# Kernel optimization log

Hardware: AMD Instinct MI355X
Metric: run time of the kernel (lower is better)

Reference implementation:

```python
import jax, jax.numpy as jnp
import numpy as np

B, T, C, A, H = 2048, 2048, 8, 27, 8  # batch, timesteps, conv in-channels, n attrs, hidden nodes
KEEP = 0.9  # dropout rate 0.1


def setup_inputs() -> dict:
    key = jax.random.key(0)
    ks = jax.random.split(key, 10)
    uni = lambda k, s: jax.random.uniform(k, s, jnp.float32, -0.05, 0.05)  # keras RandomUniform default
    # inverted dropout masks (values 0 or 1/keep); the original reuses the same seed
    # for both attrs dropouts and the same seed for both hidden dropouts -> shared masks
    mask_attrs = jax.random.bernoulli(ks[8], KEEP, (B, A)).astype(jnp.float32) / KEEP
    mask_hidden = jax.random.bernoulli(ks[9], KEEP, (B, H)).astype(jnp.float32) / KEEP
    return {
        "x": jax.random.normal(ks[0], (B, T, C), jnp.float32),
        "attrs": jax.random.normal(ks[1], (B, A), jnp.float32),
        "c2_weight_w1": uni(ks[2], (A, H)),
        "c2_weight_b1": jnp.zeros((H,), jnp.float32),
        "c2_weight_w2": uni(ks[3], (H, C)),
        "c2_weight_b2": jnp.zeros((C,), jnp.float32),
        "c2_bias_w1": uni(ks[4], (A, H)),
        "c2_bias_b1": jnp.zeros((H,), jnp.float32),
        "c2_bias_w2": uni(ks[5], (H, 1)),
        "c2_bias_b2": jnp.zeros((1,), jnp.float32),
        "mask_attrs": mask_attrs,
        "mask_hidden": mask_hidden,
    }


def reference(x, attrs, c2_weight_w1, c2_weight_b1, c2_weight_w2, c2_weight_b2,
              c2_bias_w1, c2_bias_b1, c2_bias_w2, c2_bias_b2,
              mask_attrs, mask_hidden):
    a = attrs * mask_attrs  # [B, A] shared dropout (same seed in both branches)
    # per-sample conv kernel (kernel_size=1, so just a [B, C] vector)
    hw = jax.nn.relu(a @ c2_weight_w1 + c2_weight_b1) * mask_hidden  # [B, H]
    kernel = jnp.tanh(hw @ c2_weight_w2 + c2_weight_b2)              # [B, C]
    # per-sample bias
    hb = jax.nn.relu(a @ c2_bias_w1 + c2_bias_b1) * mask_hidden      # [B, H]
    bias = jnp.tanh(hb @ c2_bias_w2 + c2_bias_b2)                    # [B, 1]
    # kernel-size-1 valid conv == per-sample channel contraction, batched across B
    y = jnp.einsum('btc,bc->bt', x, kernel) + bias                   # [B, T]
    return jax.nn.elu(y)[..., None]                                  # [B, T, 1]
```

## Files before the change

kernel.cpp:

```cpp
#include <hip/hip_runtime.h>

#define BB 2048
#define TT 2048
#define CC 8
#define AA 27
#define HH 8

__global__ __launch_bounds__(256) void mlp_kernel(
    const float* __restrict__ attrs,
    const float* __restrict__ w1,
    const float* __restrict__ b1,
    const float* __restrict__ w2,
    const float* __restrict__ b2,
    const float* __restrict__ bw1,
    const float* __restrict__ bb1,
    const float* __restrict__ bw2,
    const float* __restrict__ bb2,
    const float* __restrict__ mask_attrs,
    const float* __restrict__ mask_hidden,
    float* __restrict__ ker,
    float* __restrict__ bias)
{
    const int tid = threadIdx.x;
    const int s   = tid >> 3;
    const int h   = tid & 7;
    const int b   = blockIdx.x * 32 + s;

    __shared__ float s_hw[32][HH];
    __shared__ float s_hb[32][HH];

    {
        float hw = b1[h];
        float hb = bb1[h];
        const float* ab = attrs      + b * AA;
        const float* mb = mask_attrs + b * AA;
        #pragma unroll
        for (int i = 0; i < AA; ++i) {
            const float a = ab[i] * mb[i];
            hw = fmaf(a, w1 [i * HH + h], hw);
            hb = fmaf(a, bw1[i * HH + h], hb);
        }
        const float mh = mask_hidden[b * HH + h];
        s_hw[s][h] = fmaxf(hw, 0.0f) * mh;
        s_hb[s][h] = fmaxf(hb, 0.0f) * mh;
    }
    __syncthreads();

    {
        const int c = h;
        float acc = b2[c];
        #pragma unroll
        for (int j = 0; j < HH; ++j)
            acc = fmaf(s_hw[s][j], w2[j * CC + c], acc);
        ker[b * CC + c] = tanhf(acc);
        if (c == 0) {
            float accb = bb2[0];
            #pragma unroll
            for (int j = 0; j < HH; ++j)
                accb = fmaf(s_hb[s][j], bw2[j], accb);
            bias[b] = tanhf(accb);
        }
    }
}

__global__ __launch_bounds__(256) void stream_kernel(
    const float* __restrict__ x,
    const float* __restrict__ ker,
    const float* __restrict__ bias,
    float* __restrict__ out)
{
    const int idx = blockIdx.x * 256 + threadIdx.x;
    const int b   = idx >> 11;

    const float4* xp = reinterpret_cast<const float4*>(x + (size_t)idx * CC);
    const float4 x0 = xp[0];
    const float4 x1 = xp[1];

    const float4* kp = reinterpret_cast<const float4*>(ker + b * CC);
    const float4 k0 = kp[0];
    const float4 k1 = kp[1];
    float y = bias[b];

    y = fmaf(x0.x, k0.x, y);
    y = fmaf(x0.y, k0.y, y);
    y = fmaf(x0.z, k0.z, y);
    y = fmaf(x0.w, k0.w, y);
    y = fmaf(x1.x, k1.x, y);
    y = fmaf(x1.y, k1.y, y);
    y = fmaf(x1.z, k1.z, y);
    y = fmaf(x1.w, k1.w, y);
    out[idx] = (y > 0.0f) ? y : expm1f(y);
}

extern "C" void kernel_launch(void* const* d_in, const int* in_sizes, int n_in,
                              void* d_out, int out_size, void* d_ws, size_t ws_size,
                              hipStream_t stream) {
    const float* x    = (const float*)d_in[0];
    const float* at   = (const float*)d_in[1];
    const float* w1   = (const float*)d_in[2];
    const float* b1   = (const float*)d_in[3];
    const float* w2   = (const float*)d_in[4];
    const float* b2   = (const float*)d_in[5];
    const float* bw1  = (const float*)d_in[6];
    const float* bb1  = (const float*)d_in[7];
    const float* bw2  = (const float*)d_in[8];
    const float* bb2  = (const float*)d_in[9];
    const float* ma   = (const float*)d_in[10];
    const float* mh   = (const float*)d_in[11];
    float* out = (float*)d_out;

    float* ker  = (float*)d_ws;
    float* bias = (float*)d_ws + BB * CC;

    mlp_kernel<<<BB / 32, 256, 0, stream>>>(
        at, w1, b1, w2, b2, bw1, bb1, bw2, bb2, ma, mh, ker, bias);

    const int total  = BB * TT;
    stream_kernel<<<total / 256, 256, 0, stream>>>(x, ker, bias, out);
}
```

Before: 213.9 us.

## Fuse per-sample MLP into streaming conv kernel with per-block recompute

```diff
diff --git a/kernel.cpp b/kernel.cpp
--- a/kernel.cpp
+++ b/kernel.cpp
@@ -6,7 +6,8 @@
 #define AA 27
 #define HH 8
 
-__global__ __launch_bounds__(256) void mlp_kernel(
+__global__ __launch_bounds__(256) void fused_kernel(
+    const float* __restrict__ x,
     const float* __restrict__ attrs,
     const float* __restrict__ w1,
     const float* __restrict__ b1,
@@ -18,18 +19,19 @@
     const float* __restrict__ bb2,
     const float* __restrict__ mask_attrs,
     const float* __restrict__ mask_hidden,
-    float* __restrict__ ker,
-    float* __restrict__ bias)
+    float* __restrict__ out)
 {
     const int tid = threadIdx.x;
-    const int s   = tid >> 3;
-    const int h   = tid & 7;
-    const int b   = blockIdx.x * 32 + s;
+    const int blk = blockIdx.x;
+    const int b   = blk >> 1;
 
-    __shared__ float s_hw[32][HH];
-    __shared__ float s_hb[32][HH];
+    __shared__ float s_hw[HH];
+    __shared__ float s_hb[HH];
+    __shared__ float s_ker[CC];
+    __shared__ float s_bias;
 
-    {
+    if (tid < 8) {
+        const int h = tid;
         float hw = b1[h];
         float hb = bb1[h];
         const float* ab = attrs      + b * AA;
@@ -40,56 +42,48 @@
             hw = fmaf(a, w1 [i * HH + h], hw);
             hb = fmaf(a, bw1[i * HH + h], hb);
         }
-        const float mh = mask_hidden[b * HH + h];
-        s_hw[s][h] = fmaxf(hw, 0.0f) * mh;
-        s_hb[s][h] = fmaxf(hb, 0.0f) * mh;
+        const float mh_ = mask_hidden[b * HH + h];
+        s_hw[h] = fmaxf(hw, 0.0f) * mh_;
+        s_hb[h] = fmaxf(hb, 0.0f) * mh_;
+
+        float acc = b2[h];
+        #pragma unroll
+        for (int j = 0; j < HH; ++j)
+            acc = fmaf(s_hw[j], w2[j * CC + h], acc);
+        s_ker[h] = tanhf(acc);
+        if (h == 0) {
+            float accb = bb2[0];
+            #pragma unroll
+            for (int j = 0; j < HH; ++j)
+                accb = fmaf(s_hb[j], bw2[j], accb);
+            s_bias = tanhf(accb);
+        }
     }
     __syncthreads();
 
-    {
-        const int c = h;
-        float acc = b2[c];
-        #pragma unroll
-        for (int j = 0; j < HH; ++j)
-            acc = fmaf(s_hw[s][j], w2[j * CC + c], acc);
-        ker[b * CC + c] = tanhf(acc);
-        if (c == 0) {
-            float accb = bb2[0];
-            #pragma unroll
-            for (int j = 0; j < HH; ++j)
-                accb = fmaf(s_hb[s][j], bw2[j], accb);
-            bias[b] = tanhf(accb);
-        }
+    float k[CC];
+    #pragma unroll
+    for (int c = 0; c < CC; ++c) k[c] = s_ker[c];
+    const float bias = s_bias;
+
+    const size_t base = (size_t)blk * 1024;
+    #pragma unroll
+    for (int kk = 0; kk < 4; ++kk) {
+        const size_t idx = base + (size_t)kk * 256 + tid;
+        const float4* xp = reinterpret_cast<const float4*>(x + idx * CC);
+        const float4 x0 = xp[0];
+        const float4 x1 = xp[1];
+        float y = bias;
+        y = fmaf(x0.x, k[0], y);
+        y = fmaf(x0.y, k[1], y);
+        y = fmaf(x0.z, k[2], y);
+        y = fmaf(x0.w, k[3], y);
+        y = fmaf(x1.x, k[4], y);
+        y = fmaf(x1.y, k[5], y);
+        y = fmaf(x1.z, k[6], y);
+        y = fmaf(x1.w, k[7], y);
+        out[idx] = (y > 0.0f) ? y : expm1f(y);
     }
-}
-
-__global__ __launch_bounds__(256) void stream_kernel(
-    const float* __restrict__ x,
-    const float* __restrict__ ker,
-    const float* __restrict__ bias,
-    float* __restrict__ out)
-{
-    const int idx = blockIdx.x * 256 + threadIdx.x;
-    const int b   = idx >> 11;
-
-    const float4* xp = reinterpret_cast<const float4*>(x + (size_t)idx * CC);
-    const float4 x0 = xp[0];
-    const float4 x1 = xp[1];
-
-    const float4* kp = reinterpret_cast<const float4*>(ker + b * CC);
-    const float4 k0 = kp[0];
-    const float4 k1 = kp[1];
-    float y = bias[b];
-
-    y = fmaf(x0.x, k0.x, y);
-    y = fmaf(x0.y, k0.y, y);
-    y = fmaf(x0.z, k0.z, y);
-    y = fmaf(x0.w, k0.w, y);
-    y = fmaf(x1.x, k1.x, y);
-    y = fmaf(x1.y, k1.y, y);
-    y = fmaf(x1.z, k1.z, y);
-    y = fmaf(x1.w, k1.w, y);
-    out[idx] = (y > 0.0f) ? y : expm1f(y);
 }
 
 extern "C" void kernel_launch(void* const* d_in, const int* in_sizes, int n_in,
@@ -109,12 +103,7 @@
     const float* mh   = (const float*)d_in[11];
     float* out = (float*)d_out;
 
-    float* ker  = (float*)d_ws;
-    float* bias = (float*)d_ws + BB * CC;
-
-    mlp_kernel<<<BB / 32, 256, 0, stream>>>(
-        at, w1, b1, w2, b2, bw1, bb1, bw2, bb2, ma, mh, ker, bias);
-
-    const int total  = BB * TT;
-    stream_kernel<<<total / 256, 256, 0, stream>>>(x, ker, bias, out);
+    const int total = BB * TT;
+    fused_kernel<<<total / 1024, 256, 0, stream>>>(
+        x, at, w1, b1, w2, b2, bw1, bb1, bw2, bb2, ma, mh, out);
 }
```

After: 215.1 us. About the same (+0.6%).
